# Kernel tuning notes

Hardware: AMD Instinct MI355X
Metric: run time of the kernel (lower is better)

## Reference

```python
import jax, jax.numpy as jnp
import numpy as np

NEG_INF = -1.0e9  # matches masked_fill value in the torch module


def setup_inputs() -> dict:
    key = jax.random.key(0)
    ks = jax.random.split(key, 5)
    B, Tx = 32, 1024
    enc_hid, dec_hid, attn = 1024, 1024, 1024
    dec_hidden = jax.random.normal(ks[0], (B, dec_hid), dtype=jnp.float32)
    enc_outputs = jax.random.normal(ks[1], (B, Tx, enc_hid), dtype=jnp.float32)
    mask = jax.random.randint(ks[2], (B, Tx), 0, 2, dtype=jnp.int32)
    # ensure at least one real position per row (avoid all-masked softmax)
    mask = mask.at[:, 0].set(1)
    # nn.Linear params: weight [out, in], bias [out]
    W_w = jax.random.normal(ks[3], (attn, enc_hid + dec_hid), dtype=jnp.float32) * (1.0 / np.sqrt(enc_hid + dec_hid))
    W_b = jnp.zeros((attn,), dtype=jnp.float32)
    v_w = jax.random.normal(ks[4], (1, attn), dtype=jnp.float32) * (1.0 / np.sqrt(attn))
    return {"dec_hidden": dec_hidden, "enc_outputs": enc_outputs, "mask": mask,
            "W_w": W_w, "W_b": W_b, "v_w": v_w}


def reference(dec_hidden, enc_outputs, mask, W_w, W_b, v_w):
    # dec_hidden: [B, D], enc_outputs: [B, Tx, E], mask: [B, Tx]
    B, Tx, E = enc_outputs.shape
    D = dec_hidden.shape[-1]
    # Split W into decoder and encoder halves to avoid materializing the concat:
    # W([h; e]) = h @ W_dec^T + e @ W_enc^T + b
    W_dec = W_w[:, :D]   # [attn, D]
    W_enc = W_w[:, D:]   # [attn, E]
    dec_proj = jnp.einsum('bd,ad->ba', dec_hidden, W_dec)       # [B, attn]
    enc_proj = jnp.einsum('bte,ae->bta', enc_outputs, W_enc)    # [B, Tx, attn]
    energy = jnp.tanh(dec_proj[:, None, :] + enc_proj + W_b)    # [B, Tx, attn]
    scores = jnp.einsum('bta,a->bt', energy, v_w[0])            # [B, Tx]
    scores = jnp.where(mask == 0, NEG_INF, scores)
    alpha = jax.nn.softmax(scores, axis=1)                      # [B, Tx]
    context = jnp.einsum('bt,bte->be', alpha, enc_outputs)      # [B, E]
    return (context, alpha)
```

## Files before the change

### kernel.cpp

```cpp
#include <hip/hip_runtime.h>
#include <hip/hip_bf16.h>

typedef __bf16 bf16_t;
typedef __bf16 bf16x8_t __attribute__((ext_vector_type(8)));
typedef float f32x4_t __attribute__((ext_vector_type(4)));

#define NEG_BIG -1000000000.0f

__device__ __forceinline__ void gld_lds16(const void* g, void* l) {
    __builtin_amdgcn_global_load_lds((const __attribute__((address_space(1))) void*)g,
                                     (__attribute__((address_space(3))) void*)l,
                                     16, 0, 0);
}

__device__ __forceinline__ float tanh_fast(float x) {
    float e = __expf(2.0f * x);
    return 1.0f - 2.0f / (e + 1.0f);
}

__global__ void k_prep(const float* __restrict__ enc, const float* __restrict__ Ww,
                       const float* __restrict__ dec, const float* __restrict__ Wb,
                       bf16_t* __restrict__ encb, bf16_t* __restrict__ Bw,
                       float* __restrict__ bias) {
    const int bi = blockIdx.x;
    const int t = threadIdx.x;
    if (bi < 16384) {
        size_t flat = (size_t)bi * 2048 + t * 8;
        float4 f0 = *(const float4*)(enc + flat);
        float4 f1 = *(const float4*)(enc + flat + 4);
        bf16x8_t v;
        v[0] = (bf16_t)f0.x; v[1] = (bf16_t)f0.y; v[2] = (bf16_t)f0.z; v[3] = (bf16_t)f0.w;
        v[4] = (bf16_t)f1.x; v[5] = (bf16_t)f1.y; v[6] = (bf16_t)f1.z; v[7] = (bf16_t)f1.w;
        *(bf16x8_t*)(encb + flat) = v;
    } else if (bi < 16896) {
        size_t flat = (size_t)(bi - 16384) * 2048 + t * 8;
        int a = (int)(flat >> 10), e = (int)(flat & 1023);
        const float* src = Ww + (size_t)a * 2048 + 1024 + e;
        float4 f0 = *(const float4*)src;
        float4 f1 = *(const float4*)(src + 4);
        bf16x8_t v;
        v[0] = (bf16_t)f0.x; v[1] = (bf16_t)f0.y; v[2] = (bf16_t)f0.z; v[3] = (bf16_t)f0.w;
        v[4] = (bf16_t)f1.x; v[5] = (bf16_t)f1.y; v[6] = (bf16_t)f1.z; v[7] = (bf16_t)f1.w;
        *(bf16x8_t*)(Bw + flat) = v;
    } else {
        __shared__ float wrow[1024];
        int a = bi - 16896;
        *(float4*)(wrow + t * 4) = *(const float4*)(Ww + (size_t)a * 2048 + t * 4);
        __syncthreads();
        int b = t >> 3, j = t & 7;
        const float* dp = dec + b * 1024 + j * 128;
        const float* wp = wrow + j * 128;
        float s = 0.0f;
#pragma unroll 8
        for (int i = 0; i < 128; i += 4) {
            float4 dv = *(const float4*)(dp + i);
            float4 wv = *(const float4*)(wp + i);
            s += dv.x * wv.x + dv.y * wv.y + dv.z * wv.z + dv.w * wv.w;
        }
        s += __shfl_xor(s, 1);
        s += __shfl_xor(s, 2);
        s += __shfl_xor(s, 4);
        if (j == 0) bias[b * 1024 + a] = s + Wb[a];
    }
}

__global__ __launch_bounds__(256) void k_gemm_score(
    const bf16_t* __restrict__ A, const bf16_t* __restrict__ Bw,
    const float* __restrict__ bias, const float* __restrict__ v,
    float* __restrict__ scores) {
    __shared__ __attribute__((aligned(16))) bf16_t As[128 * 32];
    __shared__ __attribute__((aligned(16))) bf16_t Bs[128 * 32];

    const int tid = threadIdx.x;
    const int lane = tid & 63;
    const int wid = tid >> 6;
    const int wm = wid >> 1, wn = wid & 1;
    const int bm = blockIdx.x;
    const int bn = blockIdx.y;
    const int rsel = lane & 15, kg = lane >> 4;

    f32x4_t acc[4][4] = {};

    const int c0 = wid * 2;
    const int rr = lane >> 2;
    const int bj = (lane & 3) ^ ((lane >> 3) & 3);
    const bf16_t* asrc0 = A  + (size_t)(bm * 128 + c0 * 16 + rr) * 1024 + bj * 8;
    const bf16_t* asrc1 = asrc0 + (size_t)16 * 1024;
    const bf16_t* bsrc0 = Bw + (size_t)(bn * 128 + c0 * 16 + rr) * 1024 + bj * 8;
    const bf16_t* bsrc1 = bsrc0 + (size_t)16 * 1024;

    for (int kt = 0; kt < 32; ++kt) {
        const int k0 = kt * 32;
        gld_lds16(asrc0 + k0, As + c0 * 512);
        gld_lds16(asrc1 + k0, As + (c0 + 1) * 512);
        gld_lds16(bsrc0 + k0, Bs + c0 * 512);
        gld_lds16(bsrc1 + k0, Bs + (c0 + 1) * 512);
        __syncthreads();
        bf16x8_t af[4], bf[4];
        const int ksw = (kg ^ ((rsel >> 1) & 3)) * 8;
#pragma unroll
        for (int fm = 0; fm < 4; ++fm)
            af[fm] = *(const bf16x8_t*)(As + (wm * 64 + fm * 16 + rsel) * 32 + ksw);
#pragma unroll
        for (int fn = 0; fn < 4; ++fn)
            bf[fn] = *(const bf16x8_t*)(Bs + (wn * 64 + fn * 16 + rsel) * 32 + ksw);
#pragma unroll
        for (int fm = 0; fm < 4; ++fm)
#pragma unroll
            for (int fn = 0; fn < 4; ++fn)
                acc[fm][fn] = __builtin_amdgcn_mfma_f32_16x16x32_bf16(af[fm], bf[fn], acc[fm][fn], 0, 0, 0);
        __syncthreads();
    }

    const int b = bm >> 3;
    float bias_l[4], v_l[4];
#pragma unroll
    for (int fn = 0; fn < 4; ++fn) {
        int a = bn * 128 + wn * 64 + fn * 16 + rsel;
        bias_l[fn] = bias[b * 1024 + a];
        v_l[fn] = v[a];
    }
    float part[16];
#pragma unroll
    for (int fm = 0; fm < 4; ++fm)
#pragma unroll
        for (int r = 0; r < 4; ++r) {
            float p = 0.0f;
#pragma unroll
            for (int fn = 0; fn < 4; ++fn) {
                float x = acc[fm][fn][r] + bias_l[fn];
                p += tanh_fast(x) * v_l[fn];
            }
            part[fm * 4 + r] = p;
        }
#pragma unroll
    for (int k = 0; k < 16; ++k) {
        part[k] += __shfl_xor(part[k], 1);
        part[k] += __shfl_xor(part[k], 2);
        part[k] += __shfl_xor(part[k], 4);
        part[k] += __shfl_xor(part[k], 8);
    }
    const int mrow0 = bm * 128 + wm * 64 + kg * 4;
#pragma unroll
    for (int k = 0; k < 16; ++k) {
        if (rsel == k) {
            int fm = k >> 2, r = k & 3;
            atomicAdd(&scores[mrow0 + fm * 16 + r], part[k]);
        }
    }
}

__global__ void k_softmax(const float* __restrict__ scores, const int* __restrict__ mask,
                          float* __restrict__ alpha) {
    __shared__ float red[4];
    __shared__ float red2[4];
    int b = blockIdx.x, t = threadIdx.x;
    float4 s = *(const float4*)(scores + b * 1024 + t * 4);
    int4 m = *(const int4*)(mask + b * 1024 + t * 4);
    float v0 = m.x ? s.x : NEG_BIG;
    float v1 = m.y ? s.y : NEG_BIG;
    float v2 = m.z ? s.z : NEG_BIG;
    float v3 = m.w ? s.w : NEG_BIG;
    float mx = fmaxf(fmaxf(v0, v1), fmaxf(v2, v3));
#pragma unroll
    for (int o = 1; o < 64; o <<= 1) mx = fmaxf(mx, __shfl_xor(mx, o));
    if ((t & 63) == 0) red[t >> 6] = mx;
    __syncthreads();
    mx = fmaxf(fmaxf(red[0], red[1]), fmaxf(red[2], red[3]));
    float e0 = m.x ? __expf(v0 - mx) : 0.0f;
    float e1 = m.y ? __expf(v1 - mx) : 0.0f;
    float e2 = m.z ? __expf(v2 - mx) : 0.0f;
    float e3 = m.w ? __expf(v3 - mx) : 0.0f;
    float sum = e0 + e1 + e2 + e3;
#pragma unroll
    for (int o = 1; o < 64; o <<= 1) sum += __shfl_xor(sum, o);
    if ((t & 63) == 0) red2[t >> 6] = sum;
    __syncthreads();
    float inv = 1.0f / (red2[0] + red2[1] + red2[2] + red2[3]);
    float4 out = {e0 * inv, e1 * inv, e2 * inv, e3 * inv};
    *(float4*)(alpha + b * 1024 + t * 4) = out;
}

__global__ void k_ctx_part(const float* __restrict__ enc, const float* __restrict__ alpha,
                           float* __restrict__ part) {
    int chunk = blockIdx.x;
    int b = blockIdx.y;
    int t = threadIdx.x;
    int e = t * 4;
    const float* ap = alpha + b * 1024 + chunk * 32;
    const float* ep = enc + ((size_t)b * 1024 + chunk * 32) * 1024 + e;
    float ax = 0.f, ay = 0.f, az = 0.f, aw = 0.f;
#pragma unroll 4
    for (int i = 0; i < 32; ++i) {
        float a = ap[i];
        float4 x = *(const float4*)(ep + (size_t)i * 1024);
        ax += a * x.x; ay += a * x.y; az += a * x.z; aw += a * x.w;
    }
    float4 o = {ax, ay, az, aw};
    *(float4*)(part + ((size_t)chunk * 32 + b) * 1024 + e) = o;
}

__global__ void k_ctx_reduce(const float* __restrict__ part, float* __restrict__ ctx) {
    int b = blockIdx.x, t = threadIdx.x;
    int e = t * 4;
    float ax = 0.f, ay = 0.f, az = 0.f, aw = 0.f;
#pragma unroll 8
    for (int c = 0; c < 32; ++c) {
        float4 x = *(const float4*)(part + ((size_t)c * 32 + b) * 1024 + e);
        ax += x.x; ay += x.y; az += x.z; aw += x.w;
    }
    float4 o = {ax, ay, az, aw};
    *(float4*)(ctx + b * 1024 + e) = o;
}

extern "C" void kernel_launch(void* const* d_in, const int* in_sizes, int n_in,
                              void* d_out, int out_size, void* d_ws, size_t ws_size,
                              hipStream_t stream) {
    const float* dec  = (const float*)d_in[0];
    const float* enc  = (const float*)d_in[1];
    const int*   mask = (const int*)d_in[2];
    const float* Ww   = (const float*)d_in[3];
    const float* Wb   = (const float*)d_in[4];
    const float* vw   = (const float*)d_in[5];
    float* out = (float*)d_out;

    char* ws = (char*)d_ws;
    bf16_t* encb  = (bf16_t*)ws;
    bf16_t* Bw    = (bf16_t*)(ws + 67108864);
    float*  bias  = (float*)(ws + 69206016);
    float*  score = (float*)(ws + 69337088);
    float*  part  = (float*)(ws + 69468160);

    hipMemsetAsync(score, 0, 32768 * sizeof(float), stream);

    k_prep<<<17920, 256, 0, stream>>>(enc, Ww, dec, Wb, encb, Bw, bias);
    k_gemm_score<<<dim3(256, 8), 256, 0, stream>>>(encb, Bw, bias, vw, score);
    k_softmax<<<32, 256, 0, stream>>>(score, mask, out + 32768);
    k_ctx_part<<<dim3(32, 32), 256, 0, stream>>>(enc, out + 32768, part);
    k_ctx_reduce<<<32, 256, 0, stream>>>(part, out);
}
```

Before: 349.6 us.

## Double GEMM K-tile, read bf16 encoder copy for context, fold score memset

The GEMM K tile grows from 32 to 64, with an 8-way XOR swizzle, which halves the number of barrier-separated iterations. The context kernel now reads the bf16 copy of the encoder outputs instead of the fp32 original, halving the bytes read from memory, and splits each chunk into two partial sums. The reduce kernel sums twice as many partials to match. The score-buffer memset moves into extra blocks of the prep kernel, removing one launch. Using bf16 encoder values for the context lowers its precision compared with the fp32 reference.

```diff
diff --git a/kernel.cpp b/kernel.cpp
--- a/kernel.cpp
+++ b/kernel.cpp
@@ -21,7 +21,7 @@
 __global__ void k_prep(const float* __restrict__ enc, const float* __restrict__ Ww,
                        const float* __restrict__ dec, const float* __restrict__ Wb,
                        bf16_t* __restrict__ encb, bf16_t* __restrict__ Bw,
-                       float* __restrict__ bias) {
+                       float* __restrict__ bias, float* __restrict__ score) {
     const int bi = blockIdx.x;
     const int t = threadIdx.x;
     if (bi < 16384) {
@@ -42,7 +42,7 @@
         v[0] = (bf16_t)f0.x; v[1] = (bf16_t)f0.y; v[2] = (bf16_t)f0.z; v[3] = (bf16_t)f0.w;
         v[4] = (bf16_t)f1.x; v[5] = (bf16_t)f1.y; v[6] = (bf16_t)f1.z; v[7] = (bf16_t)f1.w;
         *(bf16x8_t*)(Bw + flat) = v;
-    } else {
+    } else if (bi < 17920) {
         __shared__ float wrow[1024];
         int a = bi - 16896;
         *(float4*)(wrow + t * 4) = *(const float4*)(Ww + (size_t)a * 2048 + t * 4);
@@ -61,6 +61,9 @@
         s += __shfl_xor(s, 2);
         s += __shfl_xor(s, 4);
         if (j == 0) bias[b * 1024 + a] = s + Wb[a];
+    } else {
+        float4 z = {0.f, 0.f, 0.f, 0.f};
+        *(float4*)(score + (size_t)(bi - 17920) * 1024 + t * 4) = z;
     }
 }
 
@@ -68,8 +71,8 @@
     const bf16_t* __restrict__ A, const bf16_t* __restrict__ Bw,
     const float* __restrict__ bias, const float* __restrict__ v,
     float* __restrict__ scores) {
-    __shared__ __attribute__((aligned(16))) bf16_t As[128 * 32];
-    __shared__ __attribute__((aligned(16))) bf16_t Bs[128 * 32];
+    __shared__ __attribute__((aligned(16))) bf16_t As[128 * 64];
+    __shared__ __attribute__((aligned(16))) bf16_t Bs[128 * 64];
 
     const int tid = threadIdx.x;
     const int lane = tid & 63;
@@ -81,34 +84,39 @@
 
     f32x4_t acc[4][4] = {};
 
-    const int c0 = wid * 2;
-    const int rr = lane >> 2;
-    const int bj = (lane & 3) ^ ((lane >> 3) & 3);
-    const bf16_t* asrc0 = A  + (size_t)(bm * 128 + c0 * 16 + rr) * 1024 + bj * 8;
-    const bf16_t* asrc1 = asrc0 + (size_t)16 * 1024;
-    const bf16_t* bsrc0 = Bw + (size_t)(bn * 128 + c0 * 16 + rr) * 1024 + bj * 8;
-    const bf16_t* bsrc1 = bsrc0 + (size_t)16 * 1024;
-
-    for (int kt = 0; kt < 32; ++kt) {
-        const int k0 = kt * 32;
-        gld_lds16(asrc0 + k0, As + c0 * 512);
-        gld_lds16(asrc1 + k0, As + (c0 + 1) * 512);
-        gld_lds16(bsrc0 + k0, Bs + c0 * 512);
-        gld_lds16(bsrc1 + k0, Bs + (c0 + 1) * 512);
+    const int c0 = wid * 4;
+    const int rr = lane >> 3;
+    const int ju = (lane & 7) ^ rr;
+    const bf16_t* asrc = A  + (size_t)(bm * 128 + c0 * 8 + rr) * 1024 + ju * 8;
+    const bf16_t* bsrc = Bw + (size_t)(bn * 128 + c0 * 8 + rr) * 1024 + ju * 8;
+
+    for (int kt = 0; kt < 16; ++kt) {
+        const int k0 = kt * 64;
+#pragma unroll
+        for (int c = 0; c < 4; ++c) {
+            gld_lds16(asrc + (size_t)c * 8 * 1024 + k0, As + (c0 + c) * 512);
+            gld_lds16(bsrc + (size_t)c * 8 * 1024 + k0, Bs + (c0 + c) * 512);
+        }
         __syncthreads();
-        bf16x8_t af[4], bf[4];
-        const int ksw = (kg ^ ((rsel >> 1) & 3)) * 8;
-#pragma unroll
-        for (int fm = 0; fm < 4; ++fm)
-            af[fm] = *(const bf16x8_t*)(As + (wm * 64 + fm * 16 + rsel) * 32 + ksw);
-#pragma unroll
-        for (int fn = 0; fn < 4; ++fn)
-            bf[fn] = *(const bf16x8_t*)(Bs + (wn * 64 + fn * 16 + rsel) * 32 + ksw);
-#pragma unroll
-        for (int fm = 0; fm < 4; ++fm)
-#pragma unroll
-            for (int fn = 0; fn < 4; ++fn)
-                acc[fm][fn] = __builtin_amdgcn_mfma_f32_16x16x32_bf16(af[fm], bf[fn], acc[fm][fn], 0, 0, 0);
+#pragma unroll
+        for (int s = 0; s < 2; ++s) {
+            bf16x8_t af[4], bf[4];
+#pragma unroll
+            for (int fm = 0; fm < 4; ++fm) {
+                int row = wm * 64 + fm * 16 + rsel;
+                af[fm] = *(const bf16x8_t*)(As + row * 64 + (((s * 4 + kg) ^ (row & 7)) * 8));
+            }
+#pragma unroll
+            for (int fn = 0; fn < 4; ++fn) {
+                int row = wn * 64 + fn * 16 + rsel;
+                bf[fn] = *(const bf16x8_t*)(Bs + row * 64 + (((s * 4 + kg) ^ (row & 7)) * 8));
+            }
+#pragma unroll
+            for (int fm = 0; fm < 4; ++fm)
+#pragma unroll
+                for (int fn = 0; fn < 4; ++fn)
+                    acc[fm][fn] = __builtin_amdgcn_mfma_f32_16x16x32_bf16(af[fm], bf[fn], acc[fm][fn], 0, 0, 0);
+        }
         __syncthreads();
     }
 
@@ -181,23 +189,27 @@
     *(float4*)(alpha + b * 1024 + t * 4) = out;
 }
 
-__global__ void k_ctx_part(const float* __restrict__ enc, const float* __restrict__ alpha,
+__global__ void k_ctx_part(const bf16_t* __restrict__ encb, const float* __restrict__ alpha,
                            float* __restrict__ part) {
     int chunk = blockIdx.x;
     int b = blockIdx.y;
     int t = threadIdx.x;
-    int e = t * 4;
+    int j = t >> 7;
+    int e = (t & 127) * 8;
     const float* ap = alpha + b * 1024 + chunk * 32;
-    const float* ep = enc + ((size_t)b * 1024 + chunk * 32) * 1024 + e;
-    float ax = 0.f, ay = 0.f, az = 0.f, aw = 0.f;
-#pragma unroll 4
-    for (int i = 0; i < 32; ++i) {
+    const bf16_t* ep = encb + ((size_t)b * 1024 + chunk * 32) * 1024 + e;
+    float acc[8] = {};
+    for (int i = j; i < 32; i += 2) {
         float a = ap[i];
-        float4 x = *(const float4*)(ep + (size_t)i * 1024);
-        ax += a * x.x; ay += a * x.y; az += a * x.z; aw += a * x.w;
-    }
-    float4 o = {ax, ay, az, aw};
-    *(float4*)(part + ((size_t)chunk * 32 + b) * 1024 + e) = o;
+        bf16x8_t x = *(const bf16x8_t*)(ep + (size_t)i * 1024);
+#pragma unroll
+        for (int q = 0; q < 8; ++q) acc[q] += a * (float)x[q];
+    }
+    float4 o0 = {acc[0], acc[1], acc[2], acc[3]};
+    float4 o1 = {acc[4], acc[5], acc[6], acc[7]};
+    float* dst = part + ((size_t)(chunk * 2 + j) * 32 + b) * 1024 + e;
+    *(float4*)dst = o0;
+    *(float4*)(dst + 4) = o1;
 }
 
 __global__ void k_ctx_reduce(const float* __restrict__ part, float* __restrict__ ctx) {
@@ -205,7 +217,7 @@
     int e = t * 4;
     float ax = 0.f, ay = 0.f, az = 0.f, aw = 0.f;
 #pragma unroll 8
-    for (int c = 0; c < 32; ++c) {
+    for (int c = 0; c < 64; ++c) {
         float4 x = *(const float4*)(part + ((size_t)c * 32 + b) * 1024 + e);
         ax += x.x; ay += x.y; az += x.z; aw += x.w;
     }
@@ -231,11 +243,9 @@
     float*  score = (float*)(ws + 69337088);
     float*  part  = (float*)(ws + 69468160);
 
-    hipMemsetAsync(score, 0, 32768 * sizeof(float), stream);
-
-    k_prep<<<17920, 256, 0, stream>>>(enc, Ww, dec, Wb, encb, Bw, bias);
+    k_prep<<<17952, 256, 0, stream>>>(enc, Ww, dec, Wb, encb, Bw, bias, score);
     k_gemm_score<<<dim3(256, 8), 256, 0, stream>>>(encb, Bw, bias, vw, score);
     k_softmax<<<32, 256, 0, stream>>>(score, mask, out + 32768);
-    k_ctx_part<<<dim3(32, 32), 256, 0, stream>>>(enc, out + 32768, part);
+    k_ctx_part<<<dim3(32, 32), 256, 0, stream>>>(encb, out + 32768, part);
     k_ctx_reduce<<<32, 256, 0, stream>>>(part, out);
 }
```

Result: no change. 355.0 us (+1.5%).

## Fuse fp32-to-bf16 encoder conversion into GEMM and softmax into context kernel

Applied to the files above, without the earlier changes.

Drops the separate pass that converts the 128MB fp32 encoder tensor to bf16 and writes 64MB back. The GEMM now loads fp32 rows, converts them in registers and stores swizzled bf16 into LDS, in place of the async global-to-LDS copy. Softmax is recomputed inside each context-partial block, and the score zeroing moves into the prep kernel in place of the memset. The trade-off is that the GEMM reads twice the A bytes per tile (each tile is re-read by 8 column blocks) through synchronous register loads, and the softmax is computed redundantly 32 times per row.

```diff
diff --git a/kernel.cpp b/kernel.cpp
--- a/kernel.cpp
+++ b/kernel.cpp
@@ -18,22 +18,13 @@
     return 1.0f - 2.0f / (e + 1.0f);
 }
 
-__global__ void k_prep(const float* __restrict__ enc, const float* __restrict__ Ww,
-                       const float* __restrict__ dec, const float* __restrict__ Wb,
-                       bf16_t* __restrict__ encb, bf16_t* __restrict__ Bw,
-                       float* __restrict__ bias) {
+__global__ void k_prep(const float* __restrict__ Ww, const float* __restrict__ dec,
+                       const float* __restrict__ Wb, bf16_t* __restrict__ Bw,
+                       float* __restrict__ bias, float* __restrict__ score) {
     const int bi = blockIdx.x;
     const int t = threadIdx.x;
-    if (bi < 16384) {
+    if (bi < 512) {
         size_t flat = (size_t)bi * 2048 + t * 8;
-        float4 f0 = *(const float4*)(enc + flat);
-        float4 f1 = *(const float4*)(enc + flat + 4);
-        bf16x8_t v;
-        v[0] = (bf16_t)f0.x; v[1] = (bf16_t)f0.y; v[2] = (bf16_t)f0.z; v[3] = (bf16_t)f0.w;
-        v[4] = (bf16_t)f1.x; v[5] = (bf16_t)f1.y; v[6] = (bf16_t)f1.z; v[7] = (bf16_t)f1.w;
-        *(bf16x8_t*)(encb + flat) = v;
-    } else if (bi < 16896) {
-        size_t flat = (size_t)(bi - 16384) * 2048 + t * 8;
         int a = (int)(flat >> 10), e = (int)(flat & 1023);
         const float* src = Ww + (size_t)a * 2048 + 1024 + e;
         float4 f0 = *(const float4*)src;
@@ -42,9 +33,9 @@
         v[0] = (bf16_t)f0.x; v[1] = (bf16_t)f0.y; v[2] = (bf16_t)f0.z; v[3] = (bf16_t)f0.w;
         v[4] = (bf16_t)f1.x; v[5] = (bf16_t)f1.y; v[6] = (bf16_t)f1.z; v[7] = (bf16_t)f1.w;
         *(bf16x8_t*)(Bw + flat) = v;
-    } else {
+    } else if (bi < 1536) {
         __shared__ float wrow[1024];
-        int a = bi - 16896;
+        int a = bi - 512;
         *(float4*)(wrow + t * 4) = *(const float4*)(Ww + (size_t)a * 2048 + t * 4);
         __syncthreads();
         int b = t >> 3, j = t & 7;
@@ -61,11 +52,14 @@
         s += __shfl_xor(s, 2);
         s += __shfl_xor(s, 4);
         if (j == 0) bias[b * 1024 + a] = s + Wb[a];
+    } else {
+        float4 z = {0.f, 0.f, 0.f, 0.f};
+        *(float4*)(score + (size_t)(bi - 1536) * 1024 + t * 4) = z;
     }
 }
 
 __global__ __launch_bounds__(256) void k_gemm_score(
-    const bf16_t* __restrict__ A, const bf16_t* __restrict__ Bw,
+    const float* __restrict__ enc, const bf16_t* __restrict__ Bw,
     const float* __restrict__ bias, const float* __restrict__ v,
     float* __restrict__ scores) {
     __shared__ __attribute__((aligned(16))) bf16_t As[128 * 32];
@@ -81,20 +75,37 @@
 
     f32x4_t acc[4][4] = {};
 
+    const int ar = tid >> 2;
+    const int aq = tid & 3;
+    const int asw = (tid >> 3) & 3;
+    const size_t arow0 = (size_t)(bm * 128 + ar) * 1024;
+    const size_t arow1 = (size_t)(bm * 128 + 64 + ar) * 1024;
+
     const int c0 = wid * 2;
-    const int rr = lane >> 2;
     const int bj = (lane & 3) ^ ((lane >> 3) & 3);
-    const bf16_t* asrc0 = A  + (size_t)(bm * 128 + c0 * 16 + rr) * 1024 + bj * 8;
-    const bf16_t* asrc1 = asrc0 + (size_t)16 * 1024;
-    const bf16_t* bsrc0 = Bw + (size_t)(bn * 128 + c0 * 16 + rr) * 1024 + bj * 8;
+    const bf16_t* bsrc0 = Bw + (size_t)(bn * 128 + c0 * 16 + (lane >> 2)) * 1024 + bj * 8;
     const bf16_t* bsrc1 = bsrc0 + (size_t)16 * 1024;
 
     for (int kt = 0; kt < 32; ++kt) {
         const int k0 = kt * 32;
-        gld_lds16(asrc0 + k0, As + c0 * 512);
-        gld_lds16(asrc1 + k0, As + (c0 + 1) * 512);
         gld_lds16(bsrc0 + k0, Bs + c0 * 512);
         gld_lds16(bsrc1 + k0, Bs + (c0 + 1) * 512);
+        {
+            const float* s0 = enc + arow0 + k0 + aq * 8;
+            float4 f0 = *(const float4*)s0;
+            float4 f1 = *(const float4*)(s0 + 4);
+            bf16x8_t val;
+            val[0] = (bf16_t)f0.x; val[1] = (bf16_t)f0.y; val[2] = (bf16_t)f0.z; val[3] = (bf16_t)f0.w;
+            val[4] = (bf16_t)f1.x; val[5] = (bf16_t)f1.y; val[6] = (bf16_t)f1.z; val[7] = (bf16_t)f1.w;
+            *(bf16x8_t*)(As + ar * 32 + (aq ^ asw) * 8) = val;
+            const float* s1 = enc + arow1 + k0 + aq * 8;
+            float4 g0 = *(const float4*)s1;
+            float4 g1 = *(const float4*)(s1 + 4);
+            bf16x8_t val2;
+            val2[0] = (bf16_t)g0.x; val2[1] = (bf16_t)g0.y; val2[2] = (bf16_t)g0.z; val2[3] = (bf16_t)g0.w;
+            val2[4] = (bf16_t)g1.x; val2[5] = (bf16_t)g1.y; val2[6] = (bf16_t)g1.z; val2[7] = (bf16_t)g1.w;
+            *(bf16x8_t*)(As + (64 + ar) * 32 + (aq ^ asw) * 8) = val2;
+        }
         __syncthreads();
         bf16x8_t af[4], bf[4];
         const int ksw = (kg ^ ((rsel >> 1) & 3)) * 8;
@@ -150,11 +161,16 @@
     }
 }
 
-__global__ void k_softmax(const float* __restrict__ scores, const int* __restrict__ mask,
-                          float* __restrict__ alpha) {
+__global__ void k_ctx(const float* __restrict__ enc, const float* __restrict__ scores,
+                      const int* __restrict__ mask, float* __restrict__ alpha_out,
+                      float* __restrict__ part) {
     __shared__ float red[4];
     __shared__ float red2[4];
-    int b = blockIdx.x, t = threadIdx.x;
+    __shared__ float sal[1024];
+    const int chunk = blockIdx.x;
+    const int b = blockIdx.y;
+    const int t = threadIdx.x;
+
     float4 s = *(const float4*)(scores + b * 1024 + t * 4);
     int4 m = *(const int4*)(mask + b * 1024 + t * 4);
     float v0 = m.x ? s.x : NEG_BIG;
@@ -177,18 +193,15 @@
     if ((t & 63) == 0) red2[t >> 6] = sum;
     __syncthreads();
     float inv = 1.0f / (red2[0] + red2[1] + red2[2] + red2[3]);
-    float4 out = {e0 * inv, e1 * inv, e2 * inv, e3 * inv};
-    *(float4*)(alpha + b * 1024 + t * 4) = out;
-}
-
-__global__ void k_ctx_part(const float* __restrict__ enc, const float* __restrict__ alpha,
-                           float* __restrict__ part) {
-    int chunk = blockIdx.x;
-    int b = blockIdx.y;
-    int t = threadIdx.x;
-    int e = t * 4;
-    const float* ap = alpha + b * 1024 + chunk * 32;
+    float4 al = {e0 * inv, e1 * inv, e2 * inv, e3 * inv};
+    *(float4*)(sal + t * 4) = al;
+    if (t >= chunk * 8 && t < chunk * 8 + 8)
+        *(float4*)(alpha_out + b * 1024 + t * 4) = al;
+    __syncthreads();
+
+    const int e = t * 4;
     const float* ep = enc + ((size_t)b * 1024 + chunk * 32) * 1024 + e;
+    const float* ap = sal + chunk * 32;
     float ax = 0.f, ay = 0.f, az = 0.f, aw = 0.f;
 #pragma unroll 4
     for (int i = 0; i < 32; ++i) {
@@ -225,17 +238,13 @@
     float* out = (float*)d_out;
 
     char* ws = (char*)d_ws;
-    bf16_t* encb  = (bf16_t*)ws;
-    bf16_t* Bw    = (bf16_t*)(ws + 67108864);
-    float*  bias  = (float*)(ws + 69206016);
-    float*  score = (float*)(ws + 69337088);
-    float*  part  = (float*)(ws + 69468160);
-
-    hipMemsetAsync(score, 0, 32768 * sizeof(float), stream);
-
-    k_prep<<<17920, 256, 0, stream>>>(enc, Ww, dec, Wb, encb, Bw, bias);
-    k_gemm_score<<<dim3(256, 8), 256, 0, stream>>>(encb, Bw, bias, vw, score);
-    k_softmax<<<32, 256, 0, stream>>>(score, mask, out + 32768);
-    k_ctx_part<<<dim3(32, 32), 256, 0, stream>>>(enc, out + 32768, part);
+    bf16_t* Bw    = (bf16_t*)ws;
+    float*  bias  = (float*)(ws + 2097152);
+    float*  score = (float*)(ws + 2228224);
+    float*  part  = (float*)(ws + 2359296);
+
+    k_prep<<<1568, 256, 0, stream>>>(Ww, dec, Wb, Bw, bias, score);
+    k_gemm_score<<<dim3(256, 8), 256, 0, stream>>>(enc, Bw, bias, vw, score);
+    k_ctx<<<dim3(32, 32), 256, 0, stream>>>(enc, score, mask, out + 32768, part);
     k_ctx_reduce<<<32, 256, 0, stream>>>(part, out);
 }
```

After: 349.6 us. About the same (-0.0%).

## Fuse softmax into context kernel, read bf16 encoder copy, fold memset into prep

Applied to the files above, without the earlier changes.

Each context block now recomputes the row softmax from the scores and writes only its slice of alpha, which removes the separate softmax launch. It then reduces over the bf16 encoder copy instead of the fp32 input, halving the bytes read for the context. The scores memset becomes extra blocks in the prep kernel, and the GEMM grid is linearised with a grouped block order to improve L2 reuse of the weight tiles. Context precision drops because the weighted sum now uses bf16-rounded encoder values, and the partial buffer doubles to 64 chunks.

```diff
diff --git a/kernel.cpp b/kernel.cpp
--- a/kernel.cpp
+++ b/kernel.cpp
@@ -21,7 +21,7 @@
 __global__ void k_prep(const float* __restrict__ enc, const float* __restrict__ Ww,
                        const float* __restrict__ dec, const float* __restrict__ Wb,
                        bf16_t* __restrict__ encb, bf16_t* __restrict__ Bw,
-                       float* __restrict__ bias) {
+                       float* __restrict__ bias, float* __restrict__ score) {
     const int bi = blockIdx.x;
     const int t = threadIdx.x;
     if (bi < 16384) {
@@ -42,7 +42,7 @@
         v[0] = (bf16_t)f0.x; v[1] = (bf16_t)f0.y; v[2] = (bf16_t)f0.z; v[3] = (bf16_t)f0.w;
         v[4] = (bf16_t)f1.x; v[5] = (bf16_t)f1.y; v[6] = (bf16_t)f1.z; v[7] = (bf16_t)f1.w;
         *(bf16x8_t*)(Bw + flat) = v;
-    } else {
+    } else if (bi < 17920) {
         __shared__ float wrow[1024];
         int a = bi - 16896;
         *(float4*)(wrow + t * 4) = *(const float4*)(Ww + (size_t)a * 2048 + t * 4);
@@ -61,6 +61,9 @@
         s += __shfl_xor(s, 2);
         s += __shfl_xor(s, 4);
         if (j == 0) bias[b * 1024 + a] = s + Wb[a];
+    } else {
+        float4 z = {0.f, 0.f, 0.f, 0.f};
+        *(float4*)(score + (size_t)(bi - 17920) * 1024 + t * 4) = z;
     }
 }
 
@@ -75,8 +78,9 @@
     const int lane = tid & 63;
     const int wid = tid >> 6;
     const int wm = wid >> 1, wn = wid & 1;
-    const int bm = blockIdx.x;
-    const int bn = blockIdx.y;
+    const int lin = blockIdx.x;
+    const int bm = (lin & 7) + ((lin >> 6) << 3);
+    const int bn = (lin >> 3) & 7;
     const int rsel = lane & 15, kg = lane >> 4;
 
     f32x4_t acc[4][4] = {};
@@ -150,11 +154,16 @@
     }
 }
 
-__global__ void k_softmax(const float* __restrict__ scores, const int* __restrict__ mask,
-                          float* __restrict__ alpha) {
+__global__ void k_ctx(const bf16_t* __restrict__ encb, const float* __restrict__ scores,
+                      const int* __restrict__ mask, float* __restrict__ alpha_out,
+                      float* __restrict__ part) {
     __shared__ float red[4];
     __shared__ float red2[4];
-    int b = blockIdx.x, t = threadIdx.x;
+    __shared__ float sal[1024];
+    const int chunk = blockIdx.x;
+    const int b = blockIdx.y;
+    const int t = threadIdx.x;
+
     float4 s = *(const float4*)(scores + b * 1024 + t * 4);
     int4 m = *(const int4*)(mask + b * 1024 + t * 4);
     float v0 = m.x ? s.x : NEG_BIG;
@@ -177,27 +186,28 @@
     if ((t & 63) == 0) red2[t >> 6] = sum;
     __syncthreads();
     float inv = 1.0f / (red2[0] + red2[1] + red2[2] + red2[3]);
-    float4 out = {e0 * inv, e1 * inv, e2 * inv, e3 * inv};
-    *(float4*)(alpha + b * 1024 + t * 4) = out;
-}
-
-__global__ void k_ctx_part(const float* __restrict__ enc, const float* __restrict__ alpha,
-                           float* __restrict__ part) {
-    int chunk = blockIdx.x;
-    int b = blockIdx.y;
-    int t = threadIdx.x;
-    int e = t * 4;
-    const float* ap = alpha + b * 1024 + chunk * 32;
-    const float* ep = enc + ((size_t)b * 1024 + chunk * 32) * 1024 + e;
-    float ax = 0.f, ay = 0.f, az = 0.f, aw = 0.f;
-#pragma unroll 4
-    for (int i = 0; i < 32; ++i) {
+    float4 al = {e0 * inv, e1 * inv, e2 * inv, e3 * inv};
+    *(float4*)(sal + t * 4) = al;
+    if (t >= chunk * 8 && t < chunk * 8 + 8)
+        *(float4*)(alpha_out + b * 1024 + t * 4) = al;
+    __syncthreads();
+
+    const int j = t >> 7;
+    const int e = (t & 127) * 8;
+    const bf16_t* ep = encb + ((size_t)b * 1024 + chunk * 32) * 1024 + e;
+    const float* ap = sal + chunk * 32;
+    float acc[8] = {};
+    for (int i = j; i < 32; i += 2) {
         float a = ap[i];
-        float4 x = *(const float4*)(ep + (size_t)i * 1024);
-        ax += a * x.x; ay += a * x.y; az += a * x.z; aw += a * x.w;
-    }
-    float4 o = {ax, ay, az, aw};
-    *(float4*)(part + ((size_t)chunk * 32 + b) * 1024 + e) = o;
+        bf16x8_t x = *(const bf16x8_t*)(ep + (size_t)i * 1024);
+#pragma unroll
+        for (int q = 0; q < 8; ++q) acc[q] += a * (float)x[q];
+    }
+    float4 o0 = {acc[0], acc[1], acc[2], acc[3]};
+    float4 o1 = {acc[4], acc[5], acc[6], acc[7]};
+    float* dst = part + ((size_t)(chunk * 2 + j) * 32 + b) * 1024 + e;
+    *(float4*)dst = o0;
+    *(float4*)(dst + 4) = o1;
 }
 
 __global__ void k_ctx_reduce(const float* __restrict__ part, float* __restrict__ ctx) {
@@ -205,7 +215,7 @@
     int e = t * 4;
     float ax = 0.f, ay = 0.f, az = 0.f, aw = 0.f;
 #pragma unroll 8
-    for (int c = 0; c < 32; ++c) {
+    for (int c = 0; c < 64; ++c) {
         float4 x = *(const float4*)(part + ((size_t)c * 32 + b) * 1024 + e);
         ax += x.x; ay += x.y; az += x.z; aw += x.w;
     }
@@ -231,11 +241,8 @@
     float*  score = (float*)(ws + 69337088);
     float*  part  = (float*)(ws + 69468160);
 
-    hipMemsetAsync(score, 0, 32768 * sizeof(float), stream);
-
-    k_prep<<<17920, 256, 0, stream>>>(enc, Ww, dec, Wb, encb, Bw, bias);
-    k_gemm_score<<<dim3(256, 8), 256, 0, stream>>>(encb, Bw, bias, vw, score);
-    k_softmax<<<32, 256, 0, stream>>>(score, mask, out + 32768);
-    k_ctx_part<<<dim3(32, 32), 256, 0, stream>>>(enc, out + 32768, part);
+    k_prep<<<17952, 256, 0, stream>>>(enc, Ww, dec, Wb, encb, Bw, bias, score);
+    k_gemm_score<<<2048, 256, 0, stream>>>(encb, Bw, bias, vw, score);
+    k_ctx<<<dim3(32, 32), 256, 0, stream>>>(encb, score, mask, out + 32768, part);
     k_ctx_reduce<<<32, 256, 0, stream>>>(part, out);
 }
```

Measured after the change: 341.5 us. 1.02x faster.
